# Optimization experiments

Measured on AMD Instinct MI355X. Metric: run time of the kernel, lower is better.

The kernel has to match this reference:

```python
import jax, jax.numpy as jnp
import numpy as np

D_MODEL = 1024
NUM_HEADS = 16
D_K = D_MODEL // NUM_HEADS


def setup_inputs() -> dict:
    key = jax.random.key(0)
    ks = jax.random.split(key, 11)
    B, S = 2, 2048
    scale = 1.0 / np.sqrt(D_MODEL)
    inp = {
        'Q': jax.random.normal(ks[0], (B, S, D_MODEL), dtype=jnp.float32),
        'K': jax.random.normal(ks[1], (B, S, D_MODEL), dtype=jnp.float32),
        'V': jax.random.normal(ks[2], (B, S, D_MODEL), dtype=jnp.float32),
        'Wq': jax.random.normal(ks[3], (D_MODEL, D_MODEL), dtype=jnp.float32) * scale,
        'bq': jax.random.normal(ks[4], (D_MODEL,), dtype=jnp.float32) * scale,
        'Wk': jax.random.normal(ks[5], (D_MODEL, D_MODEL), dtype=jnp.float32) * scale,
        'bk': jax.random.normal(ks[6], (D_MODEL,), dtype=jnp.float32) * scale,
        'Wv': jax.random.normal(ks[7], (D_MODEL, D_MODEL), dtype=jnp.float32) * scale,
        'bv': jax.random.normal(ks[8], (D_MODEL,), dtype=jnp.float32) * scale,
        'Wo': jax.random.normal(ks[9], (D_MODEL, D_MODEL), dtype=jnp.float32) * scale,
        'bo': jax.random.normal(ks[10], (D_MODEL,), dtype=jnp.float32) * scale,
    }
    return inp


def _split_heads(x):
    B, S, _ = x.shape
    return x.reshape(B, S, NUM_HEADS, D_K).transpose(0, 2, 1, 3)  # [B,H,S,dk]


def reference(Q, K, V, Wq, bq, Wk, bk, Wv, bv, Wo, bo):
    # Linear projections (torch Linear: x @ W.T + b)
    q = _split_heads(Q @ Wq.T + bq)
    k = _split_heads(K @ Wk.T + bk)
    v = _split_heads(V @ Wv.T + bv)
    scores = jnp.einsum('bhqd,bhkd->bhqk', q, k) / jnp.sqrt(jnp.float32(D_K))
    probs = jax.nn.softmax(scores, axis=-1)
    out = jnp.einsum('bhqk,bhkd->bhqd', probs, v)  # [B,H,S,dk]
    B, H, S, dk = out.shape
    out = out.transpose(0, 2, 1, 3).reshape(B, S, D_MODEL)
    return out @ Wo.T + bo
```

## Files before the change

kernel.cpp:

```cpp
#include <hip/hip_runtime.h>
#include <hip/hip_bf16.h>

#define DEV __device__ __forceinline__

#define BATCH 2
#define SEQ   2048
#define DMODEL 1024
#define NHEAD 16
#define DK    64
#define MROWS (BATCH*SEQ)
#define KD    1024
#define GEMM_NT (KD/32)

#define QSCALE 0.18033688011112042f

typedef __attribute__((ext_vector_type(4))) float f32x4;
typedef __attribute__((ext_vector_type(8))) short s16x8;
typedef __attribute__((ext_vector_type(4))) float fvec4;
typedef __attribute__((ext_vector_type(2))) unsigned int u32x2;
typedef __attribute__((ext_vector_type(4))) unsigned int u32x4;

__device__ short g_X[3][MROWS*DMODEL];
__device__ short g_W[4][DMODEL*DMODEL];
__device__ short g_q [MROWS*DMODEL];
__device__ short g_k [MROWS*DMODEL];
__device__ short g_vt[MROWS*DMODEL];
__device__ short g_at[MROWS*DMODEL];

DEV short f2bf(float f) {
  union { __hip_bfloat16 h; short s; } u;
  u.h = __float2bfloat16(f);
  return u.s;
}

DEV unsigned int f2bf2(float lo, float hi) {
  unsigned int r;
  asm("v_cvt_pk_bf16_f32 %0, %1, %2" : "=v"(r) : "v"(lo), "v"(hi));
  return r;
}

DEV float fexp2(float x) {
  float r;
  asm("v_exp_f32 %0, %1" : "=v"(r) : "v"(x));
  return r;
}

DEV void gload_lds16(const void* g, void* l) {
  __builtin_amdgcn_global_load_lds(
      (const __attribute__((address_space(1))) void*)g,
      (__attribute__((address_space(3))) void*)l, 16, 0, 0);
}

DEV f32x4 mfma16(s16x8 a, s16x8 b, f32x4 c) {
  return __builtin_amdgcn_mfma_f32_16x16x32_bf16(a, b, c, 0, 0, 0);
}

__global__ __launch_bounds__(256) void cast3(const float* __restrict__ a,
                                             const float* __restrict__ b,
                                             const float* __restrict__ c, int n8) {
  const float* src = blockIdx.z == 0 ? a : blockIdx.z == 1 ? b : c;
  short* dst = g_X[blockIdx.z];
  int i = blockIdx.x * 256 + threadIdx.x;
  if (i < n8) {
    const fvec4* p = (const fvec4*)(src + (size_t)i*8);
    fvec4 v0 = p[0], v1 = p[1];
    u32x4 r;
    r[0] = f2bf2(v0[0], v0[1]); r[1] = f2bf2(v0[2], v0[3]);
    r[2] = f2bf2(v1[0], v1[1]); r[3] = f2bf2(v1[2], v1[3]);
    *(u32x4*)(dst + (size_t)i*8) = r;
  }
}

__global__ __launch_bounds__(256) void cast4(const float* __restrict__ a,
                                             const float* __restrict__ b,
                                             const float* __restrict__ c,
                                             const float* __restrict__ d, int n8) {
  const float* src = blockIdx.z == 0 ? a : blockIdx.z == 1 ? b
                   : blockIdx.z == 2 ? c : d;
  short* dst = g_W[blockIdx.z];
  int i = blockIdx.x * 256 + threadIdx.x;
  if (i < n8) {
    const fvec4* p = (const fvec4*)(src + (size_t)i*8);
    fvec4 v0 = p[0], v1 = p[1];
    u32x4 r;
    r[0] = f2bf2(v0[0], v0[1]); r[1] = f2bf2(v0[2], v0[3]);
    r[2] = f2bf2(v1[0], v1[1]); r[3] = f2bf2(v1[2], v1[3]);
    *(u32x4*)(dst + (size_t)i*8) = r;
  }
}

struct GemmSmem { short As[3][128*32]; short Bs[3][128*32]; };

DEV void gemm_core(GemmSmem& sm, const short* __restrict__ A,
                   const short* __restrict__ Bw, const float* __restrict__ bias,
                   void* __restrict__ outp, float scale, int mode,
                   int rowBase, int colBase) {
  const int t = threadIdx.x, l = t & 63, w = t >> 6, g = l >> 4;
  const int wr = w >> 1, wc = w & 1;

  f32x4 acc[4][4] = {};

  auto stage = [&](int buf, int k0) {
#pragma unroll
    for (int j = 0; j < 2; ++j) {
      int e = w*1024 + j*512 + l*8;
      int e2 = e ^ (((e >> 7) & 3) << 3);
      int r = e2 >> 5, c = e2 & 31;
      gload_lds16(A  + (size_t)(rowBase + r)*KD + k0 + c, &sm.As[buf][w*1024 + j*512]);
      gload_lds16(Bw + (size_t)(colBase + r)*KD + k0 + c, &sm.Bs[buf][w*1024 + j*512]);
    }
  };

  stage(0, 0);
  stage(1, 32);

  int cur = 0, nxt = 2;
  for (int i = 0; i < GEMM_NT; ++i) {
    if (i < GEMM_NT - 1) asm volatile("s_waitcnt vmcnt(4)" ::: "memory");
    else                 asm volatile("s_waitcnt vmcnt(0)" ::: "memory");
    __builtin_amdgcn_s_barrier();
    __builtin_amdgcn_sched_barrier(0);

    s16x8 a[4], b[4];
#pragma unroll
    for (int x = 0; x < 4; ++x) {
      int ra = wr*64 + x*16 + (l & 15);
      int ia = (ra*32 + g*8) ^ (((ra >> 2) & 3) << 3);
      a[x] = *(const s16x8*)&sm.As[cur][ia];
      int rb = wc*64 + x*16 + (l & 15);
      int ib = (rb*32 + g*8) ^ (((rb >> 2) & 3) << 3);
      b[x] = *(const s16x8*)&sm.Bs[cur][ib];
    }
    if (i + 2 < GEMM_NT) stage(nxt, (i + 2)*32);
    __builtin_amdgcn_sched_barrier(0);

    __builtin_amdgcn_s_setprio(1);
#pragma unroll
    for (int x = 0; x < 4; ++x)
#pragma unroll
      for (int jn = 0; jn < 4; ++jn)
        acc[x][jn] = mfma16(a[x], b[jn], acc[x][jn]);
    __builtin_amdgcn_s_setprio(0);

    cur = cur == 2 ? 0 : cur + 1;
    nxt = nxt == 2 ? 0 : nxt + 1;
  }

#pragma unroll
  for (int x = 0; x < 4; ++x) {
    int mrow0 = rowBase + wr*64 + x*16 + g*4;
#pragma unroll
    for (int jn = 0; jn < 4; ++jn) {
      int n = colBase + wc*64 + jn*16 + (l & 15);
      float bv = bias[n];
      float val[4];
#pragma unroll
      for (int r = 0; r < 4; ++r) val[r] = (acc[x][jn][r] + bv) * scale;
      if (mode == 3) {
#pragma unroll
        for (int r = 0; r < 4; ++r)
          ((float*)outp)[(size_t)(mrow0 + r)*DMODEL + n] = val[r];
      } else {
        unsigned int pk0 = f2bf2(val[0], val[1]);
        unsigned int pk1 = f2bf2(val[2], val[3]);
        int h = n >> 6, d = n & 63;
#pragma unroll
        for (int r = 0; r < 4; ++r) {
          int m = mrow0 + r;
          int b = m >> 11, s = m & 2047;
          unsigned int pk = r < 2 ? pk0 : pk1;
          short sv = (short)((r & 1) ? (pk >> 16) : (pk & 0xffff));
          if (mode == 1)
            ((short*)outp)[(((size_t)(b*NHEAD + h)*SEQ + s)*DK) + d] = sv;
          else
            ((short*)outp)[((size_t)(b*NHEAD + h)*DK + d)*SEQ + s] = sv;
        }
      }
    }
  }
}

__global__ __launch_bounds__(256, 3)
void proj_qkv(const float* __restrict__ bq, const float* __restrict__ bk,
              const float* __restrict__ bv) {
  __shared__ GemmSmem sm;
  int z = blockIdx.z;
  int orig = blockIdx.y*8 + blockIdx.x;
  int swz = (orig & 7)*32 + (orig >> 3);
  int bx = swz & 7, by = swz >> 3;
  const float* bias = z == 0 ? bq : z == 1 ? bk : bv;
  void* outp = z == 0 ? (void*)g_q : z == 1 ? (void*)g_k : (void*)g_vt;
  gemm_core(sm, g_X[z], g_W[z], bias, outp, z == 0 ? QSCALE : 1.0f,
            z == 2 ? 2 : 1, by*128, bx*128);
}

__global__ __launch_bounds__(256, 3)
void proj_out(const float* __restrict__ bo, float* __restrict__ out) {
  __shared__ GemmSmem sm;
  int orig = blockIdx.y*8 + blockIdx.x;
  int swz = (orig & 7)*32 + (orig >> 3);
  int bx = swz & 7, by = swz >> 3;
  gemm_core(sm, g_at, g_W[3], bo, out, 1.0f, 3, by*128, bx*128);
}

__global__ __launch_bounds__(512, 4)
void attn_kernel(short* __restrict__ aout) {
  __shared__ short ks[4][64*64];
  __shared__ short vs[4][64*64];

  const int t = threadIdx.x, l = t & 63, w = t >> 6, g = l >> 4;
  const int q15 = l & 15;
  const int qg = w & 3, kp = w >> 2;
  int orig = blockIdx.y*16 + blockIdx.x;
  int swz = (orig & 7)*64 + (orig >> 3);
  const int qblk = swz & 15, bh = swz >> 4;
  const int qbase = qblk * 128;
  const size_t hoff = (size_t)bh * SEQ * DK;

  auto stage_pair = [&](int pr) {
    int e = t*8;
    int e2 = e ^ (((e >> 6) & 7) << 3);
    int t0 = 2*pr, t1 = t0 + 1;
    gload_lds16(g_k + hoff + (size_t)(t0*64)*DK + e2, &ks[t0 & 3][e]);
    gload_lds16(g_k + hoff + (size_t)(t1*64)*DK + e2, &ks[t1 & 3][e]);
    gload_lds16(g_vt + hoff + (size_t)(e2 >> 6)*SEQ + t0*64 + (e2 & 63), &vs[t0 & 3][e]);
    gload_lds16(g_vt + hoff + (size_t)(e2 >> 6)*SEQ + t1*64 + (e2 & 63), &vs[t1 & 3][e]);
  };

  s16x8 qf[2][2];
  {
    const short* q0 = g_q + hoff + (size_t)(qbase + qg*32 + q15)*DK;
    qf[0][0] = *(const s16x8*)(q0 + g*8);
    qf[0][1] = *(const s16x8*)(q0 + 32 + g*8);
    qf[1][0] = *(const s16x8*)(q0 + 16*DK + g*8);
    qf[1][1] = *(const s16x8*)(q0 + 16*DK + 32 + g*8);
  }
  stage_pair(0);

  float lsum[2] = {0.f, 0.f};
  f32x4 o[2][4] = {};

  for (int i = 0; i < 16; ++i) {
    asm volatile("s_waitcnt vmcnt(0)" ::: "memory");
    __builtin_amdgcn_s_barrier();
    __builtin_amdgcn_sched_barrier(0);
    if (i + 1 < 16) stage_pair(i + 1);

    const short* kb = ks[(2*i + kp) & 3];
    const short* vb = vs[(2*i + kp) & 3];

    f32x4 sc[2][4] = {};
    __builtin_amdgcn_s_setprio(1);
#pragma unroll
    for (int ni = 0; ni < 4; ++ni) {
      int row = ni*16 + q15;
      int sx = (row & 7) << 3;
      s16x8 k0 = *(const s16x8*)&kb[(row*64 + g*8) ^ sx];
      s16x8 k1 = *(const s16x8*)&kb[(row*64 + 32 + g*8) ^ sx];
      sc[0][ni] = mfma16(k0, qf[0][0], sc[0][ni]);
      sc[0][ni] = mfma16(k1, qf[0][1], sc[0][ni]);
      sc[1][ni] = mfma16(k0, qf[1][0], sc[1][ni]);
      sc[1][ni] = mfma16(k1, qf[1][1], sc[1][ni]);
    }
    __builtin_amdgcn_s_setprio(0);

    s16x8 pa[2][2];
#pragma unroll
    for (int grp = 0; grp < 2; ++grp) {
      float p[4][4];
#pragma unroll
      for (int ni = 0; ni < 4; ++ni)
#pragma unroll
        for (int r = 0; r < 4; ++r)
          p[ni][r] = fexp2(sc[grp][ni][r]);
      float s0 = (p[0][0]+p[0][1]) + (p[0][2]+p[0][3]);
      float s1 = (p[1][0]+p[1][1]) + (p[1][2]+p[1][3]);
      float s2 = (p[2][0]+p[2][1]) + (p[2][2]+p[2][3]);
      float s3 = (p[3][0]+p[3][1]) + (p[3][2]+p[3][3]);
      lsum[grp] += (s0+s1) + (s2+s3);

      unsigned pk[4][2];
#pragma unroll
      for (int ni = 0; ni < 4; ++ni) {
        pk[ni][0] = f2bf2(p[ni][0], p[ni][1]);
        pk[ni][1] = f2bf2(p[ni][2], p[ni][3]);
      }
#pragma unroll
      for (int kf = 0; kf < 2; ++kf) {
        u32x4 P4;
#pragma unroll
        for (int u = 0; u < 2; ++u) {
          unsigned x = pk[2*kf][u], y = pk[2*kf + 1][u];
          asm("v_permlane32_swap_b32 %0, %1" : "+v"(x), "+v"(y));
          asm("v_permlane16_swap_b32 %0, %1" : "+v"(x), "+v"(y));
          P4[u]     = x;
          P4[2 + u] = y;
        }
        union { u32x4 u4; s16x8 s8; } cv;
        cv.u4 = P4;
        pa[grp][kf] = cv.s8;
      }
    }

    __builtin_amdgcn_s_setprio(1);
#pragma unroll
    for (int nd = 0; nd < 4; ++nd) {
      int row = nd*16 + q15;
      int sx = (row & 7) << 3;
      s16x8 v0 = *(const s16x8*)&vb[(row*64 + g*8) ^ sx];
      s16x8 v1 = *(const s16x8*)&vb[(row*64 + 32 + g*8) ^ sx];
      o[0][nd] = mfma16(pa[0][0], v0, o[0][nd]);
      o[0][nd] = mfma16(pa[0][1], v1, o[0][nd]);
      o[1][nd] = mfma16(pa[1][0], v0, o[1][nd]);
      o[1][nd] = mfma16(pa[1][1], v1, o[1][nd]);
    }
    __builtin_amdgcn_s_setprio(0);
  }

  __syncthreads();
  float* ob = (float*)&vs[0][0];
  float* lb = (float*)&ks[0][0];
  if (kp) {
#pragma unroll
    for (int grp = 0; grp < 2; ++grp) {
#pragma unroll
      for (int nd = 0; nd < 4; ++nd)
#pragma unroll
        for (int r = 0; r < 4; ++r)
          ob[(qg*32 + grp*16 + nd*4 + r)*64 + l] = o[grp][nd][r];
      lb[(qg*2 + grp)*64 + l] = lsum[grp];
    }
  }
  __syncthreads();
  if (!kp) {
    int b = bh >> 4, h = bh & 15;
#pragma unroll
    for (int grp = 0; grp < 2; ++grp) {
#pragma unroll
      for (int nd = 0; nd < 4; ++nd)
#pragma unroll
        for (int r = 0; r < 4; ++r)
          o[grp][nd][r] += ob[(qg*32 + grp*16 + nd*4 + r)*64 + l];
      float ls = lsum[grp] + lb[(qg*2 + grp)*64 + l];
      ls += __shfl_xor(ls, 16);
      ls += __shfl_xor(ls, 32);
      float inv = 1.0f / ls;
      float iv[4];
#pragma unroll
      for (int r = 0; r < 4; ++r)
        iv[r] = __shfl(inv, (l & 48) | (g*4 + r));
#pragma unroll
      for (int nd = 0; nd < 4; ++nd) {
        int dcol = h*DK + nd*16 + q15;
#pragma unroll
        for (int r = 0; r < 4; ++r) {
          int srow = qbase + qg*32 + grp*16 + g*4 + r;
          aout[((size_t)(b*SEQ + srow))*DMODEL + dcol] = f2bf(o[grp][nd][r] * iv[r]);
        }
      }
    }
  }
}

extern "C" void kernel_launch(void* const* d_in, const int* in_sizes, int n_in,
                              void* d_out, int out_size, void* d_ws, size_t ws_size,
                              hipStream_t stream) {
  const float* Q  = (const float*)d_in[0];
  const float* K  = (const float*)d_in[1];
  const float* V  = (const float*)d_in[2];
  const float* Wq = (const float*)d_in[3];
  const float* bq = (const float*)d_in[4];
  const float* Wk = (const float*)d_in[5];
  const float* bk = (const float*)d_in[6];
  const float* Wv = (const float*)d_in[7];
  const float* bv = (const float*)d_in[8];
  const float* Wo = (const float*)d_in[9];
  const float* bo = (const float*)d_in[10];

  short* pat;
  hipGetSymbolAddress((void**)&pat, HIP_SYMBOL(g_at));

  const int nX8 = MROWS*DMODEL/8;
  const int nW8 = DMODEL*DMODEL/8;
  dim3 blk(256);

  cast3<<<dim3(nX8/256, 1, 3), blk, 0, stream>>>(Q, K, V, nX8);
  cast4<<<dim3(nW8/256, 1, 4), blk, 0, stream>>>(Wq, Wk, Wv, Wo, nW8);
  proj_qkv<<<dim3(DMODEL/128, MROWS/128, 3), blk, 0, stream>>>(bq, bk, bv);
  attn_kernel<<<dim3(SEQ/128, BATCH*NHEAD), dim3(512), 0, stream>>>(pat);
  proj_out<<<dim3(DMODEL/128, MROWS/128), blk, 0, stream>>>(bo, (float*)d_out);
}
```

Before: 134.2 us.

## Switch GEMM to double-buffered LDS with post-compute prefetch, merge cast kernels

The projection GEMM changes from a triple-buffered LDS pipeline to a double-buffered one. The next-next tile is now issued after a second barrier that follows the MFMA block, rather than overlapped between the LDS reads and the MFMAs. The smaller LDS footprint lets the launch bounds rise from 3 to 4 blocks per CU, trading less in-loop overlap and an extra barrier per iteration for higher occupancy. The two fp32-to-bf16 cast kernels are merged into one launch over 7 z-slices, which saves a launch but leaves many idle blocks in the weight slices.

New measurement: 136.4 us. About the same (+1.6%).

```diff
diff --git a/kernel.cpp b/kernel.cpp
--- a/kernel.cpp
+++ b/kernel.cpp
@@ -55,11 +55,24 @@
   return __builtin_amdgcn_mfma_f32_16x16x32_bf16(a, b, c, 0, 0, 0);
 }
 
-__global__ __launch_bounds__(256) void cast3(const float* __restrict__ a,
-                                             const float* __restrict__ b,
-                                             const float* __restrict__ c, int n8) {
-  const float* src = blockIdx.z == 0 ? a : blockIdx.z == 1 ? b : c;
-  short* dst = g_X[blockIdx.z];
+__global__ __launch_bounds__(256)
+void cast_all(const float* __restrict__ q, const float* __restrict__ k,
+              const float* __restrict__ v, const float* __restrict__ wq,
+              const float* __restrict__ wk, const float* __restrict__ wv,
+              const float* __restrict__ wo) {
+  int z = blockIdx.z;
+  const float* src;
+  short* dst;
+  int n8;
+  if (z < 3) {
+    src = z == 0 ? q : z == 1 ? k : v;
+    dst = g_X[z];
+    n8 = MROWS*DMODEL/8;
+  } else {
+    src = z == 3 ? wq : z == 4 ? wk : z == 5 ? wv : wo;
+    dst = g_W[z - 3];
+    n8 = DMODEL*DMODEL/8;
+  }
   int i = blockIdx.x * 256 + threadIdx.x;
   if (i < n8) {
     const fvec4* p = (const fvec4*)(src + (size_t)i*8);
@@ -71,25 +84,7 @@
   }
 }
 
-__global__ __launch_bounds__(256) void cast4(const float* __restrict__ a,
-                                             const float* __restrict__ b,
-                                             const float* __restrict__ c,
-                                             const float* __restrict__ d, int n8) {
-  const float* src = blockIdx.z == 0 ? a : blockIdx.z == 1 ? b
-                   : blockIdx.z == 2 ? c : d;
-  short* dst = g_W[blockIdx.z];
-  int i = blockIdx.x * 256 + threadIdx.x;
-  if (i < n8) {
-    const fvec4* p = (const fvec4*)(src + (size_t)i*8);
-    fvec4 v0 = p[0], v1 = p[1];
-    u32x4 r;
-    r[0] = f2bf2(v0[0], v0[1]); r[1] = f2bf2(v0[2], v0[3]);
-    r[2] = f2bf2(v1[0], v1[1]); r[3] = f2bf2(v1[2], v1[3]);
-    *(u32x4*)(dst + (size_t)i*8) = r;
-  }
-}
-
-struct GemmSmem { short As[3][128*32]; short Bs[3][128*32]; };
+struct GemmSmem { short As[2][128*32]; short Bs[2][128*32]; };
 
 DEV void gemm_core(GemmSmem& sm, const short* __restrict__ A,
                    const short* __restrict__ Bw, const float* __restrict__ bias,
@@ -114,13 +109,13 @@
   stage(0, 0);
   stage(1, 32);
 
-  int cur = 0, nxt = 2;
   for (int i = 0; i < GEMM_NT; ++i) {
     if (i < GEMM_NT - 1) asm volatile("s_waitcnt vmcnt(4)" ::: "memory");
     else                 asm volatile("s_waitcnt vmcnt(0)" ::: "memory");
     __builtin_amdgcn_s_barrier();
     __builtin_amdgcn_sched_barrier(0);
 
+    const int cur = i & 1;
     s16x8 a[4], b[4];
 #pragma unroll
     for (int x = 0; x < 4; ++x) {
@@ -131,8 +126,6 @@
       int ib = (rb*32 + g*8) ^ (((rb >> 2) & 3) << 3);
       b[x] = *(const s16x8*)&sm.Bs[cur][ib];
     }
-    if (i + 2 < GEMM_NT) stage(nxt, (i + 2)*32);
-    __builtin_amdgcn_sched_barrier(0);
 
     __builtin_amdgcn_s_setprio(1);
 #pragma unroll
@@ -142,8 +135,9 @@
         acc[x][jn] = mfma16(a[x], b[jn], acc[x][jn]);
     __builtin_amdgcn_s_setprio(0);
 
-    cur = cur == 2 ? 0 : cur + 1;
-    nxt = nxt == 2 ? 0 : nxt + 1;
+    __builtin_amdgcn_s_barrier();
+    __builtin_amdgcn_sched_barrier(0);
+    if (i + 2 < GEMM_NT) stage(cur, (i + 2)*32);
   }
 
 #pragma unroll
@@ -180,7 +174,7 @@
   }
 }
 
-__global__ __launch_bounds__(256, 3)
+__global__ __launch_bounds__(256, 4)
 void proj_qkv(const float* __restrict__ bq, const float* __restrict__ bk,
               const float* __restrict__ bv) {
   __shared__ GemmSmem sm;
@@ -194,7 +188,7 @@
             z == 2 ? 2 : 1, by*128, bx*128);
 }
 
-__global__ __launch_bounds__(256, 3)
+__global__ __launch_bounds__(256, 4)
 void proj_out(const float* __restrict__ bo, float* __restrict__ out) {
   __shared__ GemmSmem sm;
   int orig = blockIdx.y*8 + blockIdx.x;
@@ -381,11 +375,9 @@
   hipGetSymbolAddress((void**)&pat, HIP_SYMBOL(g_at));
 
   const int nX8 = MROWS*DMODEL/8;
-  const int nW8 = DMODEL*DMODEL/8;
   dim3 blk(256);
 
-  cast3<<<dim3(nX8/256, 1, 3), blk, 0, stream>>>(Q, K, V, nX8);
-  cast4<<<dim3(nW8/256, 1, 4), blk, 0, stream>>>(Wq, Wk, Wv, Wo, nW8);
+  cast_all<<<dim3(nX8/256, 1, 7), blk, 0, stream>>>(Q, K, V, Wq, Wk, Wv, Wo);
   proj_qkv<<<dim3(DMODEL/128, MROWS/128, 3), blk, 0, stream>>>(bq, bk, bv);
   attn_kernel<<<dim3(SEQ/128, BATCH*NHEAD), dim3(512), 0, stream>>>(pat);
   proj_out<<<dim3(DMODEL/128, MROWS/128), blk, 0, stream>>>(bo, (float*)d_out);
```
